# Kernel tuning notes

Measured on AMD Instinct MI355X. Metric: run time of the kernel, lower is better.

Reference implementation:

```python
import jax, jax.numpy as jnp
import numpy as np

B = 8192        # batch
OBS = 256       # obs_dim
ACT = 32        # action_dim -> output is 2*ACT (mu, log_std)
HID = 512       # hidden_dim
P = 8           # number of base policies (experts)
LOG_STD_MIN, LOG_STD_MAX = -5.0, 2.0


def setup_inputs() -> dict:
    key = jax.random.key(0)
    ks = jax.random.split(key, 14)
    s = 0.05
    return {
        "obs": jax.random.normal(ks[0], (B, OBS), dtype=jnp.float32),
        # gate network: obs -> HID -> HID -> P (softmax)
        "gw0": jax.random.normal(ks[1], (HID, OBS), dtype=jnp.float32) * s,
        "gb0": jnp.zeros((HID,), dtype=jnp.float32),
        "gw1": jax.random.normal(ks[2], (HID, HID), dtype=jnp.float32) * s,
        "gb1": jnp.zeros((HID,), dtype=jnp.float32),
        "gw2": jax.random.normal(ks[3], (P, HID), dtype=jnp.float32) * s,
        "gb2": jnp.zeros((P,), dtype=jnp.float32),
        # stacked expert (base-policy) trunk params, hidden_depth=2
        "ew0": jax.random.normal(ks[4], (P, HID, OBS), dtype=jnp.float32) * s,
        "eb0": jax.random.normal(ks[5], (P, HID), dtype=jnp.float32) * s,
        "ew1": jax.random.normal(ks[6], (P, HID, HID), dtype=jnp.float32) * s,
        "eb1": jax.random.normal(ks[7], (P, HID), dtype=jnp.float32) * s,
        "ew2": jax.random.normal(ks[8], (P, 2 * ACT, HID), dtype=jnp.float32) * s,
        "eb2": jax.random.normal(ks[9], (P, 2 * ACT), dtype=jnp.float32) * s,
    }


def _blend_linear(blend, W, b, x):
    # Math identical to: W_new = reshape(blend @ flatten(W,1)); bmm(W_new, x) + blend @ b
    # Contracted in the efficient order (per-expert GEMM then blend): [B,P,out] intermediate.
    y = jnp.einsum('bp,poi,bi->bo', blend, W, x, optimize=True)
    return y + blend @ b


def reference(obs, gw0, gb0, gw1, gb1, gw2, gb2, ew0, eb0, ew1, eb1, ew2, eb2):
    # gate network with softmax output
    h = jax.nn.relu(obs @ gw0.T + gb0)
    h = jax.nn.relu(h @ gw1.T + gb1)
    blend = jax.nn.softmax(h @ gw2.T + gb2, axis=-1)  # [B, P]

    # blended per-sample MLP (hidden_depth = 2)
    x = jax.nn.relu(_blend_linear(blend, ew0, eb0, obs))
    x = jax.nn.relu(_blend_linear(blend, ew1, eb1, x))
    x = _blend_linear(blend, ew2, eb2, x)  # [B, 2*ACT]

    mu, log_std = jnp.split(x, 2, axis=-1)
    log_std = jnp.tanh(log_std)
    log_std = LOG_STD_MIN + 0.5 * (LOG_STD_MAX - LOG_STD_MIN) * (log_std + 1.0)
    std = jnp.exp(log_std)
    # dist = SquashedNormal(mu, std); return its defining tensors
    return jnp.concatenate([mu, std], axis=-1)
```

## Files before the change

kernel.cpp:

```cpp
#include <hip/hip_runtime.h>
#include <hip/hip_bf16.h>
#include <cstdint>
#include <cstddef>

#define B_DIM   8192
#define OBS_DIM 256
#define ACT_DIM 32
#define HID_DIM 512
#define NEXPERT 8

typedef __attribute__((ext_vector_type(4))) float        f32x4;
typedef __attribute__((ext_vector_type(8))) short        s16x8;
typedef __attribute__((ext_vector_type(4))) unsigned int u32x4;

__device__ __forceinline__ unsigned cvt_pk_bf16(float lo, float hi) {
    unsigned r;
    asm("v_cvt_pk_bf16_f32 %0, %1, %2" : "=v"(r) : "v"(lo), "v"(hi));
    return r;
}
__device__ __forceinline__ float bf16_lo_f32(unsigned u) { return __uint_as_float(u << 16); }
__device__ __forceinline__ float bf16_hi_f32(unsigned u) { return __uint_as_float(u & 0xffff0000u); }

struct CvtArgs {
    const float*    s[7];
    unsigned short* d[7];
    int             nb[7];
};

__global__ __launch_bounds__(256) void cvt_multi(CvtArgs a) {
    int bid = blockIdx.x;
    int seg = 0, base = 0;
    while (seg < 6 && bid >= base + a.nb[seg]) { base += a.nb[seg]; ++seg; }
    int local = (bid - base) * 256 + threadIdx.x;
    const f32x4* s = (const f32x4*)a.s[seg];
    f32x4 v0 = s[local * 2 + 0];
    f32x4 v1 = s[local * 2 + 1];
    u32x4 o;
    o[0] = cvt_pk_bf16(v0[0], v0[1]);
    o[1] = cvt_pk_bf16(v0[2], v0[3]);
    o[2] = cvt_pk_bf16(v1[0], v1[1]);
    o[3] = cvt_pk_bf16(v1[2], v1[3]);
    ((u32x4*)a.d[seg])[local] = o;
}

__global__ __launch_bounds__(256) void gate_softmax(const unsigned short* __restrict__ h1,
                                                    const unsigned short* __restrict__ gw2,
                                                    const float* __restrict__ gb2,
                                                    float* __restrict__ blend) {
    const int lane = threadIdx.x & 63;
    const int wid  = threadIdx.x >> 6;
    const int row  = blockIdx.x * 4 + wid;

    u32x4 xv = *(const u32x4*)(h1 + (size_t)row * HID_DIM + lane * 8);
    float x[8];
#pragma unroll
    for (int j = 0; j < 4; ++j) {
        unsigned u   = xv[j];
        x[2 * j]     = bf16_lo_f32(u);
        x[2 * j + 1] = bf16_hi_f32(u);
    }
    float s[NEXPERT];
#pragma unroll
    for (int pp = 0; pp < NEXPERT; ++pp) {
        u32x4 wv = *(const u32x4*)(gw2 + (size_t)pp * HID_DIM + lane * 8);
        float d  = 0.f;
#pragma unroll
        for (int j = 0; j < 4; ++j) {
            unsigned u = wv[j];
            d += x[2 * j] * bf16_lo_f32(u);
            d += x[2 * j + 1] * bf16_hi_f32(u);
        }
        s[pp] = d;
    }
#pragma unroll
    for (int off = 1; off < 64; off <<= 1) {
#pragma unroll
        for (int pp = 0; pp < NEXPERT; ++pp) s[pp] += __shfl_xor(s[pp], off);
    }
    if (lane == 0) {
        float l[NEXPERT], m = -1e30f;
#pragma unroll
        for (int pp = 0; pp < NEXPERT; ++pp) { l[pp] = s[pp] + gb2[pp]; m = fmaxf(m, l[pp]); }
        float sum = 0.f;
#pragma unroll
        for (int pp = 0; pp < NEXPERT; ++pp) { l[pp] = __expf(l[pp] - m); sum += l[pp]; }
        float inv = 1.f / sum;
#pragma unroll
        for (int pp = 0; pp < NEXPERT; ++pp) blend[(size_t)row * NEXPERT + pp] = l[pp] * inv;
    }
}

template <int KIN, int NOUT>
__global__ __launch_bounds__(256, 2) void gemm_gate(const unsigned short* __restrict__ A,
                                                    const unsigned short* __restrict__ W,
                                                    const float* __restrict__ bias,
                                                    unsigned short* __restrict__ outb) {
    constexpr int BM = 128, BN = 64, BK = 64;

    __shared__ unsigned short sA[BM * BK];
    __shared__ unsigned short sB[BN * BK];

    const int t    = threadIdx.x;
    const int lane = t & 63;
    const int wid  = t >> 6;
    const int wm   = wid >> 1, wn = wid & 1;
    const int m0   = blockIdx.x * BM;
    const int n0   = blockIdx.y * BN;

    f32x4 acc[4][2];
#pragma unroll
    for (int i = 0; i < 4; ++i)
#pragma unroll
        for (int j = 0; j < 2; ++j) acc[i][j] = {0.f, 0.f, 0.f, 0.f};

#pragma unroll 1
    for (int kt = 0; kt < KIN / BK; ++kt) {
        const int ks = kt * BK;
        __syncthreads();
        const unsigned short* Wp = W + (size_t)n0 * KIN + ks;
#pragma unroll
        for (int c = 0; c < 2; ++c) {
            const int ch  = c * 256 + t;
            const int row = ch >> 3;
            const int gs  = (ch & 7) ^ (row & 7);
            __builtin_amdgcn_global_load_lds(
                (const __attribute__((address_space(1))) unsigned int*)(Wp + (size_t)row * KIN + gs * 8),
                (__attribute__((address_space(3))) unsigned int*)(sB + ch * 8), 16, 0, 0);
        }
        const unsigned short* Ap = A + (size_t)m0 * KIN + ks;
#pragma unroll
        for (int c = 0; c < 4; ++c) {
            const int ch  = c * 256 + t;
            const int row = ch >> 3;
            const int gs  = (ch & 7) ^ (row & 7);
            __builtin_amdgcn_global_load_lds(
                (const __attribute__((address_space(1))) unsigned int*)(Ap + (size_t)row * KIN + gs * 8),
                (__attribute__((address_space(3))) unsigned int*)(sA + ch * 8), 16, 0, 0);
        }
        __syncthreads();

#pragma unroll
        for (int kk = 0; kk < BK; kk += 32) {
            const int kb = kk + ((lane >> 4) << 3);
            s16x8 af[4], bfr[2];
#pragma unroll
            for (int mf = 0; mf < 4; ++mf) {
                const int row = wm * 64 + mf * 16 + (lane & 15);
                const int idx = (row * BK + kb) ^ ((row & 7) << 3);
                af[mf] = *(const s16x8*)(sA + idx);
            }
#pragma unroll
            for (int nf = 0; nf < 2; ++nf) {
                const int row = wn * 32 + nf * 16 + (lane & 15);
                const int idx = (row * BK + kb) ^ ((row & 7) << 3);
                bfr[nf] = *(const s16x8*)(sB + idx);
            }
#pragma unroll
            for (int mf = 0; mf < 4; ++mf)
#pragma unroll
                for (int nf = 0; nf < 2; ++nf)
                    acc[mf][nf] = __builtin_amdgcn_mfma_f32_16x16x32_bf16(af[mf], bfr[nf],
                                                                          acc[mf][nf], 0, 0, 0);
        }
    }

    const int cn = lane & 15;
    const int rb = (lane >> 4) << 2;
#pragma unroll
    for (int nf = 0; nf < 2; ++nf) {
        const int gn   = n0 + wn * 32 + nf * 16 + cn;
        const float bv = bias[gn];
#pragma unroll
        for (int mf = 0; mf < 4; ++mf) {
#pragma unroll
            for (int r = 0; r < 4; ++r) {
                const int gm = m0 + wm * 64 + mf * 16 + rb + r;
                float v = fmaxf(acc[mf][nf][r] + bv, 0.f);
                outb[(size_t)gm * NOUT + gn] = (unsigned short)(cvt_pk_bf16(v, v) & 0xffffu);
            }
        }
    }
}

template <int KIN, int NOUT, int BN, int TPB>
__global__ __launch_bounds__(256, 2) void gemm_moe_sk(const unsigned short* __restrict__ A,
                                                      const unsigned short* __restrict__ W,
                                                      const float* __restrict__ blend,
                                                      float* __restrict__ part) {
    constexpr int BM  = 128, BK = 64;
    constexpr int NF  = BN / 32;
    constexpr int TPE = KIN / BK;
    constexpr int NPE = (TPB >= TPE) ? TPB / TPE : 1;
    constexpr int ET  = (TPB >= TPE) ? TPE : TPB;
    static_assert((TPB % TPE == 0) || (TPE % TPB == 0), "split/expert alignment");

    __shared__ unsigned short sA[BM * BK];
    __shared__ unsigned short sB[BN * BK];

    const int t    = threadIdx.x;
    const int lane = t & 63;
    const int wid  = t >> 6;
    const int wm   = wid >> 1, wn = wid & 1;
    const int m0   = blockIdx.x * BM;
    const int n0   = blockIdx.y * BN;
    const int sp   = blockIdx.z;

    const int cn = lane & 15;
    const int rb = (lane >> 4) << 2;

    f32x4 mast[4][NF];
#pragma unroll
    for (int i = 0; i < 4; ++i)
#pragma unroll
        for (int j = 0; j < NF; ++j) mast[i][j] = {0.f, 0.f, 0.f, 0.f};

#pragma unroll 1
    for (int pe = 0; pe < NPE; ++pe) {
        const int tbase = sp * TPB + pe * ET;
        const int p     = tbase / TPE;
        const int ksb   = (tbase % TPE) * BK;

        f32x4 eacc[4][NF];
#pragma unroll
        for (int i = 0; i < 4; ++i)
#pragma unroll
            for (int j = 0; j < NF; ++j) eacc[i][j] = {0.f, 0.f, 0.f, 0.f};

        const unsigned short* Ap0 = A + (size_t)m0 * KIN + ksb;
        const unsigned short* Wp0 = W + ((size_t)p * NOUT + n0) * KIN + ksb;

#pragma unroll 1
        for (int kt = 0; kt < ET; ++kt) {
            const int ks = kt * BK;
            __syncthreads();
#pragma unroll
            for (int c = 0; c < NF; ++c) {
                const int ch  = c * 256 + t;
                const int row = ch >> 3;
                const int gs  = (ch & 7) ^ (row & 7);
                __builtin_amdgcn_global_load_lds(
                    (const __attribute__((address_space(1))) unsigned int*)(Wp0 + (size_t)row * KIN + ks + gs * 8),
                    (__attribute__((address_space(3))) unsigned int*)(sB + ch * 8), 16, 0, 0);
            }
#pragma unroll
            for (int c = 0; c < 4; ++c) {
                const int ch  = c * 256 + t;
                const int row = ch >> 3;
                const int gs  = (ch & 7) ^ (row & 7);
                __builtin_amdgcn_global_load_lds(
                    (const __attribute__((address_space(1))) unsigned int*)(Ap0 + (size_t)row * KIN + ks + gs * 8),
                    (__attribute__((address_space(3))) unsigned int*)(sA + ch * 8), 16, 0, 0);
            }
            __syncthreads();

#pragma unroll
            for (int kk = 0; kk < BK; kk += 32) {
                const int kb = kk + ((lane >> 4) << 3);
                s16x8 af[4], bfr[NF];
#pragma unroll
                for (int mf = 0; mf < 4; ++mf) {
                    const int row = wm * 64 + mf * 16 + (lane & 15);
                    const int idx = (row * BK + kb) ^ ((row & 7) << 3);
                    af[mf] = *(const s16x8*)(sA + idx);
                }
#pragma unroll
                for (int nf = 0; nf < NF; ++nf) {
                    const int row = wn * (BN / 2) + nf * 16 + (lane & 15);
                    const int idx = (row * BK + kb) ^ ((row & 7) << 3);
                    bfr[nf] = *(const s16x8*)(sB + idx);
                }
#pragma unroll
                for (int mf = 0; mf < 4; ++mf)
#pragma unroll
                    for (int nf = 0; nf < NF; ++nf)
                        eacc[mf][nf] = __builtin_amdgcn_mfma_f32_16x16x32_bf16(af[mf], bfr[nf],
                                                                               eacc[mf][nf], 0, 0, 0);
            }
        }

#pragma unroll
        for (int mf = 0; mf < 4; ++mf) {
#pragma unroll
            for (int r = 0; r < 4; ++r) {
                const int gm = m0 + wm * 64 + mf * 16 + rb + r;
                const float bl = blend[(size_t)gm * NEXPERT + p];
#pragma unroll
                for (int nf = 0; nf < NF; ++nf)
                    mast[mf][nf][r] += bl * eacc[mf][nf][r];
            }
        }
    }

    float* dst = part + (size_t)sp * B_DIM * NOUT;
#pragma unroll
    for (int mf = 0; mf < 4; ++mf) {
#pragma unroll
        for (int r = 0; r < 4; ++r) {
            const int gm = m0 + wm * 64 + mf * 16 + rb + r;
#pragma unroll
            for (int nf = 0; nf < NF; ++nf) {
                const int gn = n0 + wn * (BN / 2) + nf * 16 + cn;
                dst[(size_t)gm * NOUT + gn] = mast[mf][nf][r];
            }
        }
    }
}

template <int NS>
__global__ __launch_bounds__(256) void reduceN_relu(const float* __restrict__ part,
                                                    const float* __restrict__ blend,
                                                    const float* __restrict__ eb,
                                                    unsigned short* __restrict__ out) {
    const int tid = blockIdx.x * 256 + threadIdx.x;
    const int row = tid >> 6;
    const int c0  = (tid & 63) << 3;

    float res[8] = {0.f, 0.f, 0.f, 0.f, 0.f, 0.f, 0.f, 0.f};
#pragma unroll
    for (int s = 0; s < NS; ++s) {
        const f32x4* ps = (const f32x4*)(part + ((size_t)s * B_DIM + row) * HID_DIM + c0);
        const f32x4 a = ps[0], b = ps[1];
#pragma unroll
        for (int j = 0; j < 4; ++j) { res[j] += a[j]; res[4 + j] += b[j]; }
    }
    const f32x4* bl = (const f32x4*)(blend + (size_t)row * NEXPERT);
    const f32x4 b0 = bl[0], b1 = bl[1];
    const float blv[8] = {b0[0], b0[1], b0[2], b0[3], b1[0], b1[1], b1[2], b1[3]};
#pragma unroll
    for (int pp = 0; pp < NEXPERT; ++pp) {
        const f32x4* e = (const f32x4*)(eb + (size_t)pp * HID_DIM + c0);
        const f32x4 e0 = e[0], e1 = e[1];
#pragma unroll
        for (int j = 0; j < 4; ++j) {
            res[j]     += blv[pp] * e0[j];
            res[4 + j] += blv[pp] * e1[j];
        }
    }
    u32x4 o;
#pragma unroll
    for (int j = 0; j < 4; ++j)
        o[j] = cvt_pk_bf16(fmaxf(res[2 * j], 0.f), fmaxf(res[2 * j + 1], 0.f));
    *(u32x4*)(out + (size_t)row * HID_DIM + c0) = o;
}

__global__ __launch_bounds__(256) void reduce16_head(const float* __restrict__ part,
                                                     const float* __restrict__ blend,
                                                     const float* __restrict__ eb2,
                                                     float* __restrict__ out) {
    const int tid = blockIdx.x * 256 + threadIdx.x;
    const int row = tid >> 3;
    const int c0  = (tid & 7) << 3;

    float res[8] = {0.f, 0.f, 0.f, 0.f, 0.f, 0.f, 0.f, 0.f};
#pragma unroll
    for (int sp = 0; sp < 16; ++sp) {
        const f32x4* ps = (const f32x4*)(part + ((size_t)sp * B_DIM + row) * 64 + c0);
        const f32x4 a = ps[0], b = ps[1];
#pragma unroll
        for (int j = 0; j < 4; ++j) { res[j] += a[j]; res[4 + j] += b[j]; }
    }
    const f32x4* bl = (const f32x4*)(blend + (size_t)row * NEXPERT);
    const f32x4 b0 = bl[0], b1 = bl[1];
    const float blv[8] = {b0[0], b0[1], b0[2], b0[3], b1[0], b1[1], b1[2], b1[3]};
#pragma unroll
    for (int pp = 0; pp < NEXPERT; ++pp) {
        const f32x4* e = (const f32x4*)(eb2 + (size_t)pp * 64 + c0);
        const f32x4 e0 = e[0], e1 = e[1];
#pragma unroll
        for (int j = 0; j < 4; ++j) {
            res[j]     += blv[pp] * e0[j];
            res[4 + j] += blv[pp] * e1[j];
        }
    }
    f32x4 o0, o1;
#pragma unroll
    for (int j = 0; j < 8; ++j) {
        const int col = c0 + j;
        float v = res[j];
        if (col >= ACT_DIM) {
            const float vc = fminf(fmaxf(v, -15.f), 15.f);
            const float e2 = __expf(2.f * vc);
            const float th = (e2 - 1.f) / (e2 + 1.f);
            v = __expf(-1.5f + 3.5f * th);
        }
        if (j < 4) o0[j] = v; else o1[j - 4] = v;
    }
    f32x4* dst = (f32x4*)(out + (size_t)row * 64 + c0);
    dst[0] = o0;
    dst[1] = o1;
}

extern "C" void kernel_launch(void* const* d_in, const int* in_sizes, int n_in,
                              void* d_out, int out_size, void* d_ws, size_t ws_size,
                              hipStream_t stream) {
    const float* obs = (const float*)d_in[0];
    const float* gw0 = (const float*)d_in[1];
    const float* gb0 = (const float*)d_in[2];
    const float* gw1 = (const float*)d_in[3];
    const float* gb1 = (const float*)d_in[4];
    const float* gw2 = (const float*)d_in[5];
    const float* gb2 = (const float*)d_in[6];
    const float* ew0 = (const float*)d_in[7];
    const float* eb0 = (const float*)d_in[8];
    const float* ew1 = (const float*)d_in[9];
    const float* eb1 = (const float*)d_in[10];
    const float* ew2 = (const float*)d_in[11];
    const float* eb2 = (const float*)d_in[12];

    char* w = (char*)d_ws;
    auto alloc = [&](size_t bytes) {
        char* r = w;
        w += (bytes + 255) & ~(size_t)255;
        return r;
    };
    unsigned short* obs_bf = (unsigned short*)alloc((size_t)B_DIM * OBS_DIM * 2);
    unsigned short* gw0_bf = (unsigned short*)alloc((size_t)HID_DIM * OBS_DIM * 2);
    unsigned short* gw1_bf = (unsigned short*)alloc((size_t)HID_DIM * HID_DIM * 2);
    unsigned short* gw2_bf = (unsigned short*)alloc((size_t)NEXPERT * HID_DIM * 2);
    unsigned short* ew0_bf = (unsigned short*)alloc((size_t)NEXPERT * HID_DIM * OBS_DIM * 2);
    unsigned short* ew1_bf = (unsigned short*)alloc((size_t)NEXPERT * HID_DIM * HID_DIM * 2);
    unsigned short* ew2_bf = (unsigned short*)alloc((size_t)NEXPERT * 2 * ACT_DIM * HID_DIM * 2);
    unsigned short* h0     = (unsigned short*)alloc((size_t)B_DIM * HID_DIM * 2);
    unsigned short* h1     = (unsigned short*)alloc((size_t)B_DIM * HID_DIM * 2);
    float*          blend  = (float*)alloc((size_t)B_DIM * NEXPERT * 4);

    const size_t part4_bytes = (size_t)4 * B_DIM * HID_DIM * 4;
    const size_t part2_bytes = (size_t)2 * B_DIM * HID_DIM * 4;
    const size_t used        = (size_t)(w - (char*)d_ws);
    const bool   big         = (ws_size - used) >= part4_bytes;
    float* part = (float*)alloc(big ? part4_bytes : part2_bytes);

    CvtArgs ca;
    ca.s[0] = obs; ca.d[0] = obs_bf; ca.nb[0] = (B_DIM * OBS_DIM / 8) / 256;
    ca.s[1] = gw0; ca.d[1] = gw0_bf; ca.nb[1] = (HID_DIM * OBS_DIM / 8) / 256;
    ca.s[2] = gw1; ca.d[2] = gw1_bf; ca.nb[2] = (HID_DIM * HID_DIM / 8) / 256;
    ca.s[3] = gw2; ca.d[3] = gw2_bf; ca.nb[3] = (NEXPERT * HID_DIM / 8) / 256;
    ca.s[4] = ew0; ca.d[4] = ew0_bf; ca.nb[4] = (NEXPERT * HID_DIM * OBS_DIM / 8) / 256;
    ca.s[5] = ew1; ca.d[5] = ew1_bf; ca.nb[5] = (NEXPERT * HID_DIM * HID_DIM / 8) / 256;
    ca.s[6] = ew2; ca.d[6] = ew2_bf; ca.nb[6] = (NEXPERT * 64 * HID_DIM / 8) / 256;
    int total_blocks = 0;
    for (int i = 0; i < 7; ++i) total_blocks += ca.nb[i];
    cvt_multi<<<total_blocks, 256, 0, stream>>>(ca);

    gemm_gate<OBS_DIM, HID_DIM><<<dim3(B_DIM / 128, HID_DIM / 64), 256, 0, stream>>>(
        obs_bf, gw0_bf, gb0, h0);
    gemm_gate<HID_DIM, HID_DIM><<<dim3(B_DIM / 128, HID_DIM / 64), 256, 0, stream>>>(
        h0, gw1_bf, gb1, h1);
    gate_softmax<<<B_DIM / 4, 256, 0, stream>>>(h1, gw2_bf, gb2, blend);

    if (big) {
        gemm_moe_sk<OBS_DIM, HID_DIM, 128, 8>
            <<<dim3(B_DIM / 128, HID_DIM / 128, 4), 256, 0, stream>>>(obs_bf, ew0_bf, blend, part);
        reduceN_relu<4><<<B_DIM * 64 / 256, 256, 0, stream>>>(part, blend, eb0, h0);

        gemm_moe_sk<HID_DIM, HID_DIM, 128, 16>
            <<<dim3(B_DIM / 128, HID_DIM / 128, 4), 256, 0, stream>>>(h0, ew1_bf, blend, part);
        reduceN_relu<4><<<B_DIM * 64 / 256, 256, 0, stream>>>(part, blend, eb1, h1);
    } else {
        gemm_moe_sk<OBS_DIM, HID_DIM, 128, 16>
            <<<dim3(B_DIM / 128, HID_DIM / 128, 2), 256, 0, stream>>>(obs_bf, ew0_bf, blend, part);
        reduceN_relu<2><<<B_DIM * 64 / 256, 256, 0, stream>>>(part, blend, eb0, h0);

        gemm_moe_sk<HID_DIM, HID_DIM, 128, 32>
            <<<dim3(B_DIM / 128, HID_DIM / 128, 2), 256, 0, stream>>>(h0, ew1_bf, blend, part);
        reduceN_relu<2><<<B_DIM * 64 / 256, 256, 0, stream>>>(part, blend, eb1, h1);
    }

    gemm_moe_sk<HID_DIM, 64, 64, 4>
        <<<dim3(B_DIM / 128, 1, 16), 256, 0, stream>>>(h1, ew2_bf, blend, part);
    reduce16_head<<<B_DIM * 8 / 256, 256, 0, stream>>>(part, blend, eb2, (float*)d_out);
}
```

Measured before the change: 231.9 us.

## Use 512-thread expert GEMM blocks, always split in two, shrink head split-K

The two hidden-layer expert GEMMs move to a new 512-thread kernel with 8 waves in a 2x4 layout. Each wave now holds half as many N fragments. Both layers now always use the 2-way split that covers four experts per block, which drops the 4-way split path and halves partial-buffer traffic. The head GEMM drops from 16 to 8 splits, one expert per split, with the blend applied at store time, and its reduction shrinks to match. The change trades fewer blocks and less reduction traffic for lower parallelism per layer, and a different occupancy and register profile.

```diff
diff --git a/kernel.cpp b/kernel.cpp
--- a/kernel.cpp
+++ b/kernel.cpp
@@ -183,16 +183,165 @@
 }
 
 template <int KIN, int NOUT, int BN, int TPB>
-__global__ __launch_bounds__(256, 2) void gemm_moe_sk(const unsigned short* __restrict__ A,
-                                                      const unsigned short* __restrict__ W,
-                                                      const float* __restrict__ blend,
-                                                      float* __restrict__ part) {
+__global__ __launch_bounds__(512, 2) void gemm_moe_sk8(const unsigned short* __restrict__ A,
+                                                       const unsigned short* __restrict__ W,
+                                                       const float* __restrict__ blend,
+                                                       float* __restrict__ part) {
+    constexpr int BM  = 128, BK = 64;
+    constexpr int NF  = BN / 64;
+    constexpr int TPE = KIN / BK;
+    constexpr int NPE = (TPB >= TPE) ? TPB / TPE : 1;
+    constexpr int ET  = (TPB >= TPE) ? TPE : TPB;
+    static_assert((TPB % TPE == 0) || (TPE % TPB == 0), "split/expert alignment");
+
+    __shared__ unsigned short sA[BM * BK];
+    __shared__ unsigned short sB[BN * BK];
+
+    const int t    = threadIdx.x;
+    const int lane = t & 63;
+    const int wid  = t >> 6;
+    const int wm   = wid >> 2;
+    const int wn   = wid & 3;
+    const int m0   = blockIdx.x * BM;
+    const int n0   = blockIdx.y * BN;
+    const int sp   = blockIdx.z;
+
+    const int cn = lane & 15;
+    const int rb = (lane >> 4) << 2;
+
+    f32x4 mast[4][NF];
+    if constexpr (NPE > 1) {
+#pragma unroll
+        for (int i = 0; i < 4; ++i)
+#pragma unroll
+            for (int j = 0; j < NF; ++j) mast[i][j] = {0.f, 0.f, 0.f, 0.f};
+    }
+
+    float lastbl[4];
+
+#pragma unroll 1
+    for (int pe = 0; pe < NPE; ++pe) {
+        const int tbase = sp * TPB + pe * ET;
+        const int p     = tbase / TPE;
+        const int ksb   = (tbase % TPE) * BK;
+
+        f32x4 eacc[4][NF];
+#pragma unroll
+        for (int i = 0; i < 4; ++i)
+#pragma unroll
+            for (int j = 0; j < NF; ++j) eacc[i][j] = {0.f, 0.f, 0.f, 0.f};
+
+        const unsigned short* Ap0 = A + (size_t)m0 * KIN + ksb;
+        const unsigned short* Wp0 = W + ((size_t)p * NOUT + n0) * KIN + ksb;
+
+#pragma unroll 1
+        for (int kt = 0; kt < ET; ++kt) {
+            const int ks = kt * BK;
+            __syncthreads();
+#pragma unroll
+            for (int c = 0; c < BN * 8 / 512; ++c) {
+                const int ch  = c * 512 + t;
+                const int row = ch >> 3;
+                const int gs  = (ch & 7) ^ (row & 7);
+                __builtin_amdgcn_global_load_lds(
+                    (const __attribute__((address_space(1))) unsigned int*)(Wp0 + (size_t)row * KIN + ks + gs * 8),
+                    (__attribute__((address_space(3))) unsigned int*)(sB + ch * 8), 16, 0, 0);
+            }
+#pragma unroll
+            for (int c = 0; c < 2; ++c) {
+                const int ch  = c * 512 + t;
+                const int row = ch >> 3;
+                const int gs  = (ch & 7) ^ (row & 7);
+                __builtin_amdgcn_global_load_lds(
+                    (const __attribute__((address_space(1))) unsigned int*)(Ap0 + (size_t)row * KIN + ks + gs * 8),
+                    (__attribute__((address_space(3))) unsigned int*)(sA + ch * 8), 16, 0, 0);
+            }
+            __syncthreads();
+
+#pragma unroll
+            for (int kk = 0; kk < BK; kk += 32) {
+                const int kb = kk + ((lane >> 4) << 3);
+                s16x8 af[4], bfr[NF];
+#pragma unroll
+                for (int mf = 0; mf < 4; ++mf) {
+                    const int row = wm * 64 + mf * 16 + (lane & 15);
+                    const int idx = (row * BK + kb) ^ ((row & 7) << 3);
+                    af[mf] = *(const s16x8*)(sA + idx);
+                }
+#pragma unroll
+                for (int nf = 0; nf < NF; ++nf) {
+                    const int row = wn * (BN / 4) + nf * 16 + (lane & 15);
+                    const int idx = (row * BK + kb) ^ ((row & 7) << 3);
+                    bfr[nf] = *(const s16x8*)(sB + idx);
+                }
+#pragma unroll
+                for (int mf = 0; mf < 4; ++mf)
+#pragma unroll
+                    for (int nf = 0; nf < NF; ++nf)
+                        eacc[mf][nf] = __builtin_amdgcn_mfma_f32_16x16x32_bf16(af[mf], bfr[nf],
+                                                                               eacc[mf][nf], 0, 0, 0);
+            }
+        }
+
+        if constexpr (NPE > 1) {
+#pragma unroll
+            for (int mf = 0; mf < 4; ++mf) {
+#pragma unroll
+                for (int r = 0; r < 4; ++r) {
+                    const int gm = m0 + wm * 64 + mf * 16 + rb + r;
+                    const float bl = blend[(size_t)gm * NEXPERT + p];
+#pragma unroll
+                    for (int nf = 0; nf < NF; ++nf)
+                        mast[mf][nf][r] += bl * eacc[mf][nf][r];
+                }
+            }
+        } else {
+#pragma unroll
+            for (int mf = 0; mf < 4; ++mf) {
+                const int gm = m0 + wm * 64 + mf * 16 + rb;
+                lastbl[mf] = 0.f;
+                (void)gm;
+#pragma unroll
+                for (int r = 0; r < 4; ++r) {
+                    const float bl = blend[(size_t)(m0 + wm * 64 + mf * 16 + rb + r) * NEXPERT + p];
+#pragma unroll
+                    for (int nf = 0; nf < NF; ++nf)
+                        eacc[mf][nf][r] *= bl;
+                }
+#pragma unroll
+                for (int nf = 0; nf < NF; ++nf) mast[mf][nf] = eacc[mf][nf];
+            }
+        }
+    }
+    (void)lastbl;
+
+    float* dst = part + (size_t)sp * B_DIM * NOUT;
+#pragma unroll
+    for (int mf = 0; mf < 4; ++mf) {
+#pragma unroll
+        for (int r = 0; r < 4; ++r) {
+            const int gm = m0 + wm * 64 + mf * 16 + rb + r;
+#pragma unroll
+            for (int nf = 0; nf < NF; ++nf) {
+                const int gn = n0 + wn * (BN / 4) + nf * 16 + cn;
+                dst[(size_t)gm * NOUT + gn] = mast[mf][nf][r];
+            }
+        }
+    }
+}
+
+template <int KIN, int NOUT, int BN, int TPB>
+__global__ __launch_bounds__(256, 2) void gemm_moe_sk4(const unsigned short* __restrict__ A,
+                                                       const unsigned short* __restrict__ W,
+                                                       const float* __restrict__ blend,
+                                                       float* __restrict__ part) {
     constexpr int BM  = 128, BK = 64;
     constexpr int NF  = BN / 32;
     constexpr int TPE = KIN / BK;
     constexpr int NPE = (TPB >= TPE) ? TPB / TPE : 1;
     constexpr int ET  = (TPB >= TPE) ? TPE : TPB;
     static_assert((TPB % TPE == 0) || (TPE % TPB == 0), "split/expert alignment");
+    static_assert(NPE == 1, "sk4 is the single-expert-chunk path");
 
     __shared__ unsigned short sA[BM * BK];
     __shared__ unsigned short sB[BN * BK];
@@ -208,86 +357,65 @@
     const int cn = lane & 15;
     const int rb = (lane >> 4) << 2;
 
-    f32x4 mast[4][NF];
+    const int tbase = sp * TPB;
+    const int p     = tbase / TPE;
+    const int ksb   = (tbase % TPE) * BK;
+
+    f32x4 eacc[4][NF];
 #pragma unroll
     for (int i = 0; i < 4; ++i)
 #pragma unroll
-        for (int j = 0; j < NF; ++j) mast[i][j] = {0.f, 0.f, 0.f, 0.f};
+        for (int j = 0; j < NF; ++j) eacc[i][j] = {0.f, 0.f, 0.f, 0.f};
+
+    const unsigned short* Ap0 = A + (size_t)m0 * KIN + ksb;
+    const unsigned short* Wp0 = W + ((size_t)p * NOUT + n0) * KIN + ksb;
 
 #pragma unroll 1
-    for (int pe = 0; pe < NPE; ++pe) {
-        const int tbase = sp * TPB + pe * ET;
-        const int p     = tbase / TPE;
-        const int ksb   = (tbase % TPE) * BK;
-
-        f32x4 eacc[4][NF];
-#pragma unroll
-        for (int i = 0; i < 4; ++i)
-#pragma unroll
-            for (int j = 0; j < NF; ++j) eacc[i][j] = {0.f, 0.f, 0.f, 0.f};
-
-        const unsigned short* Ap0 = A + (size_t)m0 * KIN + ksb;
-        const unsigned short* Wp0 = W + ((size_t)p * NOUT + n0) * KIN + ksb;
-
-#pragma unroll 1
-        for (int kt = 0; kt < ET; ++kt) {
-            const int ks = kt * BK;
-            __syncthreads();
-#pragma unroll
-            for (int c = 0; c < NF; ++c) {
-                const int ch  = c * 256 + t;
-                const int row = ch >> 3;
-                const int gs  = (ch & 7) ^ (row & 7);
-                __builtin_amdgcn_global_load_lds(
-                    (const __attribute__((address_space(1))) unsigned int*)(Wp0 + (size_t)row * KIN + ks + gs * 8),
-                    (__attribute__((address_space(3))) unsigned int*)(sB + ch * 8), 16, 0, 0);
-            }
-#pragma unroll
-            for (int c = 0; c < 4; ++c) {
-                const int ch  = c * 256 + t;
-                const int row = ch >> 3;
-                const int gs  = (ch & 7) ^ (row & 7);
-                __builtin_amdgcn_global_load_lds(
-                    (const __attribute__((address_space(1))) unsigned int*)(Ap0 + (size_t)row * KIN + ks + gs * 8),
-                    (__attribute__((address_space(3))) unsigned int*)(sA + ch * 8), 16, 0, 0);
-            }
-            __syncthreads();
-
-#pragma unroll
-            for (int kk = 0; kk < BK; kk += 32) {
-                const int kb = kk + ((lane >> 4) << 3);
-                s16x8 af[4], bfr[NF];
-#pragma unroll
-                for (int mf = 0; mf < 4; ++mf) {
-                    const int row = wm * 64 + mf * 16 + (lane & 15);
-                    const int idx = (row * BK + kb) ^ ((row & 7) << 3);
-                    af[mf] = *(const s16x8*)(sA + idx);
-                }
-#pragma unroll
-                for (int nf = 0; nf < NF; ++nf) {
-                    const int row = wn * (BN / 2) + nf * 16 + (lane & 15);
-                    const int idx = (row * BK + kb) ^ ((row & 7) << 3);
-                    bfr[nf] = *(const s16x8*)(sB + idx);
-                }
-#pragma unroll
-                for (int mf = 0; mf < 4; ++mf)
-#pragma unroll
-                    for (int nf = 0; nf < NF; ++nf)
-                        eacc[mf][nf] = __builtin_amdgcn_mfma_f32_16x16x32_bf16(af[mf], bfr[nf],
-                                                                               eacc[mf][nf], 0, 0, 0);
-            }
-        }
-
-#pragma unroll
-        for (int mf = 0; mf < 4; ++mf) {
-#pragma unroll
-            for (int r = 0; r < 4; ++r) {
-                const int gm = m0 + wm * 64 + mf * 16 + rb + r;
-                const float bl = blend[(size_t)gm * NEXPERT + p];
+    for (int kt = 0; kt < ET; ++kt) {
+        const int ks = kt * BK;
+        __syncthreads();
+#pragma unroll
+        for (int c = 0; c < NF; ++c) {
+            const int ch  = c * 256 + t;
+            const int row = ch >> 3;
+            const int gs  = (ch & 7) ^ (row & 7);
+            __builtin_amdgcn_global_load_lds(
+                (const __attribute__((address_space(1))) unsigned int*)(Wp0 + (size_t)row * KIN + ks + gs * 8),
+                (__attribute__((address_space(3))) unsigned int*)(sB + ch * 8), 16, 0, 0);
+        }
+#pragma unroll
+        for (int c = 0; c < 4; ++c) {
+            const int ch  = c * 256 + t;
+            const int row = ch >> 3;
+            const int gs  = (ch & 7) ^ (row & 7);
+            __builtin_amdgcn_global_load_lds(
+                (const __attribute__((address_space(1))) unsigned int*)(Ap0 + (size_t)row * KIN + ks + gs * 8),
+                (__attribute__((address_space(3))) unsigned int*)(sA + ch * 8), 16, 0, 0);
+        }
+        __syncthreads();
+
+#pragma unroll
+        for (int kk = 0; kk < BK; kk += 32) {
+            const int kb = kk + ((lane >> 4) << 3);
+            s16x8 af[4], bfr[NF];
+#pragma unroll
+            for (int mf = 0; mf < 4; ++mf) {
+                const int row = wm * 64 + mf * 16 + (lane & 15);
+                const int idx = (row * BK + kb) ^ ((row & 7) << 3);
+                af[mf] = *(const s16x8*)(sA + idx);
+            }
+#pragma unroll
+            for (int nf = 0; nf < NF; ++nf) {
+                const int row = wn * (BN / 2) + nf * 16 + (lane & 15);
+                const int idx = (row * BK + kb) ^ ((row & 7) << 3);
+                bfr[nf] = *(const s16x8*)(sB + idx);
+            }
+#pragma unroll
+            for (int mf = 0; mf < 4; ++mf)
 #pragma unroll
                 for (int nf = 0; nf < NF; ++nf)
-                    mast[mf][nf][r] += bl * eacc[mf][nf][r];
-            }
+                    eacc[mf][nf] = __builtin_amdgcn_mfma_f32_16x16x32_bf16(af[mf], bfr[nf],
+                                                                           eacc[mf][nf], 0, 0, 0);
         }
     }
 
@@ -297,10 +425,11 @@
 #pragma unroll
         for (int r = 0; r < 4; ++r) {
             const int gm = m0 + wm * 64 + mf * 16 + rb + r;
+            const float bl = blend[(size_t)gm * NEXPERT + p];
 #pragma unroll
             for (int nf = 0; nf < NF; ++nf) {
                 const int gn = n0 + wn * (BN / 2) + nf * 16 + cn;
-                dst[(size_t)gm * NOUT + gn] = mast[mf][nf][r];
+                dst[(size_t)gm * NOUT + gn] = bl * eacc[mf][nf][r];
             }
         }
     }
@@ -343,17 +472,17 @@
     *(u32x4*)(out + (size_t)row * HID_DIM + c0) = o;
 }
 
-__global__ __launch_bounds__(256) void reduce16_head(const float* __restrict__ part,
-                                                     const float* __restrict__ blend,
-                                                     const float* __restrict__ eb2,
-                                                     float* __restrict__ out) {
+__global__ __launch_bounds__(256) void reduce8_head(const float* __restrict__ part,
+                                                    const float* __restrict__ blend,
+                                                    const float* __restrict__ eb2,
+                                                    float* __restrict__ out) {
     const int tid = blockIdx.x * 256 + threadIdx.x;
     const int row = tid >> 3;
     const int c0  = (tid & 7) << 3;
 
     float res[8] = {0.f, 0.f, 0.f, 0.f, 0.f, 0.f, 0.f, 0.f};
 #pragma unroll
-    for (int sp = 0; sp < 16; ++sp) {
+    for (int sp = 0; sp < 8; ++sp) {
         const f32x4* ps = (const f32x4*)(part + ((size_t)sp * B_DIM + row) * 64 + c0);
         const f32x4 a = ps[0], b = ps[1];
 #pragma unroll
@@ -423,12 +552,7 @@
     unsigned short* h0     = (unsigned short*)alloc((size_t)B_DIM * HID_DIM * 2);
     unsigned short* h1     = (unsigned short*)alloc((size_t)B_DIM * HID_DIM * 2);
     float*          blend  = (float*)alloc((size_t)B_DIM * NEXPERT * 4);
-
-    const size_t part4_bytes = (size_t)4 * B_DIM * HID_DIM * 4;
-    const size_t part2_bytes = (size_t)2 * B_DIM * HID_DIM * 4;
-    const size_t used        = (size_t)(w - (char*)d_ws);
-    const bool   big         = (ws_size - used) >= part4_bytes;
-    float* part = (float*)alloc(big ? part4_bytes : part2_bytes);
+    float*          part   = (float*)alloc((size_t)2 * B_DIM * HID_DIM * 4);
 
     CvtArgs ca;
     ca.s[0] = obs; ca.d[0] = obs_bf; ca.nb[0] = (B_DIM * OBS_DIM / 8) / 256;
@@ -448,25 +572,15 @@
         h0, gw1_bf, gb1, h1);
     gate_softmax<<<B_DIM / 4, 256, 0, stream>>>(h1, gw2_bf, gb2, blend);
 
-    if (big) {
-        gemm_moe_sk<OBS_DIM, HID_DIM, 128, 8>
-            <<<dim3(B_DIM / 128, HID_DIM / 128, 4), 256, 0, stream>>>(obs_bf, ew0_bf, blend, part);
-        reduceN_relu<4><<<B_DIM * 64 / 256, 256, 0, stream>>>(part, blend, eb0, h0);
-
-        gemm_moe_sk<HID_DIM, HID_DIM, 128, 16>
-            <<<dim3(B_DIM / 128, HID_DIM / 128, 4), 256, 0, stream>>>(h0, ew1_bf, blend, part);
-        reduceN_relu<4><<<B_DIM * 64 / 256, 256, 0, stream>>>(part, blend, eb1, h1);
-    } else {
-        gemm_moe_sk<OBS_DIM, HID_DIM, 128, 16>
-            <<<dim3(B_DIM / 128, HID_DIM / 128, 2), 256, 0, stream>>>(obs_bf, ew0_bf, blend, part);
-        reduceN_relu<2><<<B_DIM * 64 / 256, 256, 0, stream>>>(part, blend, eb0, h0);
-
-        gemm_moe_sk<HID_DIM, HID_DIM, 128, 32>
-            <<<dim3(B_DIM / 128, HID_DIM / 128, 2), 256, 0, stream>>>(h0, ew1_bf, blend, part);
-        reduceN_relu<2><<<B_DIM * 64 / 256, 256, 0, stream>>>(part, blend, eb1, h1);
-    }
-
-    gemm_moe_sk<HID_DIM, 64, 64, 4>
-        <<<dim3(B_DIM / 128, 1, 16), 256, 0, stream>>>(h1, ew2_bf, blend, part);
-    reduce16_head<<<B_DIM * 8 / 256, 256, 0, stream>>>(part, blend, eb2, (float*)d_out);
-}
+    gemm_moe_sk8<OBS_DIM, HID_DIM, 128, 16>
+        <<<dim3(B_DIM / 128, HID_DIM / 128, 2), 512, 0, stream>>>(obs_bf, ew0_bf, blend, part);
+    reduceN_relu<2><<<B_DIM * 64 / 256, 256, 0, stream>>>(part, blend, eb0, h0);
+
+    gemm_moe_sk8<HID_DIM, HID_DIM, 128, 32>
+        <<<dim3(B_DIM / 128, HID_DIM / 128, 2), 512, 0, stream>>>(h0, ew1_bf, blend, part);
+    reduceN_relu<2><<<B_DIM * 64 / 256, 256, 0, stream>>>(part, blend, eb1, h1);
+
+    gemm_moe_sk4<HID_DIM, 64, 64, 8>
+        <<<dim3(B_DIM / 128, 1, 8), 256, 0, stream>>>(h1, ew2_bf, blend, part);
+    reduce8_head<<<B_DIM * 8 / 256, 256, 0, stream>>>(part, blend, eb2, (float*)d_out);
+}
```

Result: slower. 247.3 us (+6.6%).

## Double-buffer LDS in gate and MoE GEMMs and reduce split-K counts

Applied to the files above, without the earlier changes.

Adds double-buffered shared memory to the gate and expert GEMMs, so the next K tile is loaded asynchronously while MFMAs run on the current one. The MoE kernel's nested per-expert loop becomes a single flat tile loop that folds the blended expert accumulator into the master accumulator at expert boundaries. The launch config is fixed to the 2-way split for the hidden layers and 8-way for the head, which drops the workspace-size branch and halves the head's reduction partials. LDS use doubles per block, which may cut occupancy, and fewer splits reduce grid parallelism.

```diff
diff --git a/kernel.cpp b/kernel.cpp
--- a/kernel.cpp
+++ b/kernel.cpp
@@ -96,9 +96,10 @@
                                                     const float* __restrict__ bias,
                                                     unsigned short* __restrict__ outb) {
     constexpr int BM = 128, BN = 64, BK = 64;
-
-    __shared__ unsigned short sA[BM * BK];
-    __shared__ unsigned short sB[BN * BK];
+    constexpr int NT = KIN / BK;
+
+    __shared__ unsigned short sA[2][BM * BK];
+    __shared__ unsigned short sB[2][BN * BK];
 
     const int t    = threadIdx.x;
     const int lane = t & 63;
@@ -107,16 +108,8 @@
     const int m0   = blockIdx.x * BM;
     const int n0   = blockIdx.y * BN;
 
-    f32x4 acc[4][2];
-#pragma unroll
-    for (int i = 0; i < 4; ++i)
-#pragma unroll
-        for (int j = 0; j < 2; ++j) acc[i][j] = {0.f, 0.f, 0.f, 0.f};
-
-#pragma unroll 1
-    for (int kt = 0; kt < KIN / BK; ++kt) {
-        const int ks = kt * BK;
-        __syncthreads();
+    auto stage = [&](int tile, int buf) {
+        const int ks = tile * BK;
         const unsigned short* Wp = W + (size_t)n0 * KIN + ks;
 #pragma unroll
         for (int c = 0; c < 2; ++c) {
@@ -125,7 +118,7 @@
             const int gs  = (ch & 7) ^ (row & 7);
             __builtin_amdgcn_global_load_lds(
                 (const __attribute__((address_space(1))) unsigned int*)(Wp + (size_t)row * KIN + gs * 8),
-                (__attribute__((address_space(3))) unsigned int*)(sB + ch * 8), 16, 0, 0);
+                (__attribute__((address_space(3))) unsigned int*)(&sB[buf][ch * 8]), 16, 0, 0);
         }
         const unsigned short* Ap = A + (size_t)m0 * KIN + ks;
 #pragma unroll
@@ -135,9 +128,23 @@
             const int gs  = (ch & 7) ^ (row & 7);
             __builtin_amdgcn_global_load_lds(
                 (const __attribute__((address_space(1))) unsigned int*)(Ap + (size_t)row * KIN + gs * 8),
-                (__attribute__((address_space(3))) unsigned int*)(sA + ch * 8), 16, 0, 0);
-        }
-        __syncthreads();
+                (__attribute__((address_space(3))) unsigned int*)(&sA[buf][ch * 8]), 16, 0, 0);
+        }
+    };
+
+    f32x4 acc[4][2];
+#pragma unroll
+    for (int i = 0; i < 4; ++i)
+#pragma unroll
+        for (int j = 0; j < 2; ++j) acc[i][j] = {0.f, 0.f, 0.f, 0.f};
+
+    stage(0, 0);
+    __syncthreads();
+    int cur = 0;
+
+#pragma unroll 1
+    for (int tile = 0; tile < NT; ++tile) {
+        if (tile + 1 < NT) stage(tile + 1, cur ^ 1);
 
 #pragma unroll
         for (int kk = 0; kk < BK; kk += 32) {
@@ -147,13 +154,13 @@
             for (int mf = 0; mf < 4; ++mf) {
                 const int row = wm * 64 + mf * 16 + (lane & 15);
                 const int idx = (row * BK + kb) ^ ((row & 7) << 3);
-                af[mf] = *(const s16x8*)(sA + idx);
+                af[mf] = *(const s16x8*)(&sA[cur][idx]);
             }
 #pragma unroll
             for (int nf = 0; nf < 2; ++nf) {
                 const int row = wn * 32 + nf * 16 + (lane & 15);
                 const int idx = (row * BK + kb) ^ ((row & 7) << 3);
-                bfr[nf] = *(const s16x8*)(sB + idx);
+                bfr[nf] = *(const s16x8*)(&sB[cur][idx]);
             }
 #pragma unroll
             for (int mf = 0; mf < 4; ++mf)
@@ -162,6 +169,8 @@
                     acc[mf][nf] = __builtin_amdgcn_mfma_f32_16x16x32_bf16(af[mf], bfr[nf],
                                                                           acc[mf][nf], 0, 0, 0);
         }
+        __syncthreads();
+        cur ^= 1;
     }
 
     const int cn = lane & 15;
@@ -190,12 +199,11 @@
     constexpr int BM  = 128, BK = 64;
     constexpr int NF  = BN / 32;
     constexpr int TPE = KIN / BK;
-    constexpr int NPE = (TPB >= TPE) ? TPB / TPE : 1;
     constexpr int ET  = (TPB >= TPE) ? TPE : TPB;
     static_assert((TPB % TPE == 0) || (TPE % TPB == 0), "split/expert alignment");
 
-    __shared__ unsigned short sA[BM * BK];
-    __shared__ unsigned short sB[BN * BK];
+    __shared__ unsigned short sA[2][BM * BK];
+    __shared__ unsigned short sB[2][BN * BK];
 
     const int t    = threadIdx.x;
     const int lane = t & 63;
@@ -207,88 +215,94 @@
 
     const int cn = lane & 15;
     const int rb = (lane >> 4) << 2;
-
-    f32x4 mast[4][NF];
+    const unsigned gbase = (unsigned)sp * TPB;
+
+    auto stage = [&](int tile, int buf) {
+        const unsigned g  = gbase + (unsigned)tile;
+        const unsigned p  = g / TPE;
+        const unsigned ko = (g % TPE) * BK;
+        const unsigned short* Wp = W + ((size_t)p * NOUT + n0) * KIN + ko;
+#pragma unroll
+        for (int c = 0; c < BN / 32; ++c) {
+            const int ch  = c * 256 + t;
+            const int row = ch >> 3;
+            const int gs  = (ch & 7) ^ (row & 7);
+            __builtin_amdgcn_global_load_lds(
+                (const __attribute__((address_space(1))) unsigned int*)(Wp + (size_t)row * KIN + gs * 8),
+                (__attribute__((address_space(3))) unsigned int*)(&sB[buf][ch * 8]), 16, 0, 0);
+        }
+        const unsigned short* Ap = A + (size_t)m0 * KIN + ko;
+#pragma unroll
+        for (int c = 0; c < 4; ++c) {
+            const int ch  = c * 256 + t;
+            const int row = ch >> 3;
+            const int gs  = (ch & 7) ^ (row & 7);
+            __builtin_amdgcn_global_load_lds(
+                (const __attribute__((address_space(1))) unsigned int*)(Ap + (size_t)row * KIN + gs * 8),
+                (__attribute__((address_space(3))) unsigned int*)(&sA[buf][ch * 8]), 16, 0, 0);
+        }
+    };
+
+    f32x4 mast[4][NF], eacc[4][NF];
 #pragma unroll
     for (int i = 0; i < 4; ++i)
 #pragma unroll
-        for (int j = 0; j < NF; ++j) mast[i][j] = {0.f, 0.f, 0.f, 0.f};
+        for (int j = 0; j < NF; ++j) {
+            mast[i][j] = {0.f, 0.f, 0.f, 0.f};
+            eacc[i][j] = {0.f, 0.f, 0.f, 0.f};
+        }
+
+    stage(0, 0);
+    __syncthreads();
+    int cur = 0;
 
 #pragma unroll 1
-    for (int pe = 0; pe < NPE; ++pe) {
-        const int tbase = sp * TPB + pe * ET;
-        const int p     = tbase / TPE;
-        const int ksb   = (tbase % TPE) * BK;
-
-        f32x4 eacc[4][NF];
-#pragma unroll
-        for (int i = 0; i < 4; ++i)
-#pragma unroll
-            for (int j = 0; j < NF; ++j) eacc[i][j] = {0.f, 0.f, 0.f, 0.f};
-
-        const unsigned short* Ap0 = A + (size_t)m0 * KIN + ksb;
-        const unsigned short* Wp0 = W + ((size_t)p * NOUT + n0) * KIN + ksb;
-
-#pragma unroll 1
-        for (int kt = 0; kt < ET; ++kt) {
-            const int ks = kt * BK;
-            __syncthreads();
-#pragma unroll
-            for (int c = 0; c < NF; ++c) {
-                const int ch  = c * 256 + t;
-                const int row = ch >> 3;
-                const int gs  = (ch & 7) ^ (row & 7);
-                __builtin_amdgcn_global_load_lds(
-                    (const __attribute__((address_space(1))) unsigned int*)(Wp0 + (size_t)row * KIN + ks + gs * 8),
-                    (__attribute__((address_space(3))) unsigned int*)(sB + ch * 8), 16, 0, 0);
-            }
-#pragma unroll
-            for (int c = 0; c < 4; ++c) {
-                const int ch  = c * 256 + t;
-                const int row = ch >> 3;
-                const int gs  = (ch & 7) ^ (row & 7);
-                __builtin_amdgcn_global_load_lds(
-                    (const __attribute__((address_space(1))) unsigned int*)(Ap0 + (size_t)row * KIN + ks + gs * 8),
-                    (__attribute__((address_space(3))) unsigned int*)(sA + ch * 8), 16, 0, 0);
-            }
-            __syncthreads();
-
-#pragma unroll
-            for (int kk = 0; kk < BK; kk += 32) {
-                const int kb = kk + ((lane >> 4) << 3);
-                s16x8 af[4], bfr[NF];
-#pragma unroll
-                for (int mf = 0; mf < 4; ++mf) {
-                    const int row = wm * 64 + mf * 16 + (lane & 15);
-                    const int idx = (row * BK + kb) ^ ((row & 7) << 3);
-                    af[mf] = *(const s16x8*)(sA + idx);
+    for (int tile = 0; tile < TPB; ++tile) {
+        if (tile + 1 < TPB) stage(tile + 1, cur ^ 1);
+
+#pragma unroll
+        for (int kk = 0; kk < BK; kk += 32) {
+            const int kb = kk + ((lane >> 4) << 3);
+            s16x8 af[4], bfr[NF];
+#pragma unroll
+            for (int mf = 0; mf < 4; ++mf) {
+                const int row = wm * 64 + mf * 16 + (lane & 15);
+                const int idx = (row * BK + kb) ^ ((row & 7) << 3);
+                af[mf] = *(const s16x8*)(&sA[cur][idx]);
+            }
+#pragma unroll
+            for (int nf = 0; nf < NF; ++nf) {
+                const int row = wn * (BN / 2) + nf * 16 + (lane & 15);
+                const int idx = (row * BK + kb) ^ ((row & 7) << 3);
+                bfr[nf] = *(const s16x8*)(&sB[cur][idx]);
+            }
+#pragma unroll
+            for (int mf = 0; mf < 4; ++mf)
+#pragma unroll
+                for (int nf = 0; nf < NF; ++nf)
+                    eacc[mf][nf] = __builtin_amdgcn_mfma_f32_16x16x32_bf16(af[mf], bfr[nf],
+                                                                           eacc[mf][nf], 0, 0, 0);
+        }
+
+        if (((tile + 1) & (ET - 1)) == 0) {
+            const unsigned p = (gbase + (unsigned)tile) / TPE;
+#pragma unroll
+            for (int mf = 0; mf < 4; ++mf) {
+#pragma unroll
+                for (int r = 0; r < 4; ++r) {
+                    const int gm = m0 + wm * 64 + mf * 16 + rb + r;
+                    const float bl = blend[(size_t)gm * NEXPERT + p];
+#pragma unroll
+                    for (int nf = 0; nf < NF; ++nf) {
+                        mast[mf][nf][r] += bl * eacc[mf][nf][r];
+                        eacc[mf][nf][r] = 0.f;
+                    }
                 }
-#pragma unroll
-                for (int nf = 0; nf < NF; ++nf) {
-                    const int row = wn * (BN / 2) + nf * 16 + (lane & 15);
-                    const int idx = (row * BK + kb) ^ ((row & 7) << 3);
-                    bfr[nf] = *(const s16x8*)(sB + idx);
-                }
-#pragma unroll
-                for (int mf = 0; mf < 4; ++mf)
-#pragma unroll
-                    for (int nf = 0; nf < NF; ++nf)
-                        eacc[mf][nf] = __builtin_amdgcn_mfma_f32_16x16x32_bf16(af[mf], bfr[nf],
-                                                                               eacc[mf][nf], 0, 0, 0);
-            }
-        }
-
-#pragma unroll
-        for (int mf = 0; mf < 4; ++mf) {
-#pragma unroll
-            for (int r = 0; r < 4; ++r) {
-                const int gm = m0 + wm * 64 + mf * 16 + rb + r;
-                const float bl = blend[(size_t)gm * NEXPERT + p];
-#pragma unroll
-                for (int nf = 0; nf < NF; ++nf)
-                    mast[mf][nf][r] += bl * eacc[mf][nf][r];
-            }
-        }
+            }
+        }
+
+        __syncthreads();
+        cur ^= 1;
     }
 
     float* dst = part + (size_t)sp * B_DIM * NOUT;
@@ -343,17 +357,17 @@
     *(u32x4*)(out + (size_t)row * HID_DIM + c0) = o;
 }
 
-__global__ __launch_bounds__(256) void reduce16_head(const float* __restrict__ part,
-                                                     const float* __restrict__ blend,
-                                                     const float* __restrict__ eb2,
-                                                     float* __restrict__ out) {
+__global__ __launch_bounds__(256) void reduce8_head(const float* __restrict__ part,
+                                                    const float* __restrict__ blend,
+                                                    const float* __restrict__ eb2,
+                                                    float* __restrict__ out) {
     const int tid = blockIdx.x * 256 + threadIdx.x;
     const int row = tid >> 3;
     const int c0  = (tid & 7) << 3;
 
     float res[8] = {0.f, 0.f, 0.f, 0.f, 0.f, 0.f, 0.f, 0.f};
 #pragma unroll
-    for (int sp = 0; sp < 16; ++sp) {
+    for (int sp = 0; sp < 8; ++sp) {
         const f32x4* ps = (const f32x4*)(part + ((size_t)sp * B_DIM + row) * 64 + c0);
         const f32x4 a = ps[0], b = ps[1];
 #pragma unroll
@@ -423,12 +437,7 @@
     unsigned short* h0     = (unsigned short*)alloc((size_t)B_DIM * HID_DIM * 2);
     unsigned short* h1     = (unsigned short*)alloc((size_t)B_DIM * HID_DIM * 2);
     float*          blend  = (float*)alloc((size_t)B_DIM * NEXPERT * 4);
-
-    const size_t part4_bytes = (size_t)4 * B_DIM * HID_DIM * 4;
-    const size_t part2_bytes = (size_t)2 * B_DIM * HID_DIM * 4;
-    const size_t used        = (size_t)(w - (char*)d_ws);
-    const bool   big         = (ws_size - used) >= part4_bytes;
-    float* part = (float*)alloc(big ? part4_bytes : part2_bytes);
+    float*          part   = (float*)alloc((size_t)2 * B_DIM * HID_DIM * 4);
 
     CvtArgs ca;
     ca.s[0] = obs; ca.d[0] = obs_bf; ca.nb[0] = (B_DIM * OBS_DIM / 8) / 256;
@@ -448,25 +457,15 @@
         h0, gw1_bf, gb1, h1);
     gate_softmax<<<B_DIM / 4, 256, 0, stream>>>(h1, gw2_bf, gb2, blend);
 
-    if (big) {
-        gemm_moe_sk<OBS_DIM, HID_DIM, 128, 8>
-            <<<dim3(B_DIM / 128, HID_DIM / 128, 4), 256, 0, stream>>>(obs_bf, ew0_bf, blend, part);
-        reduceN_relu<4><<<B_DIM * 64 / 256, 256, 0, stream>>>(part, blend, eb0, h0);
-
-        gemm_moe_sk<HID_DIM, HID_DIM, 128, 16>
-            <<<dim3(B_DIM / 128, HID_DIM / 128, 4), 256, 0, stream>>>(h0, ew1_bf, blend, part);
-        reduceN_relu<4><<<B_DIM * 64 / 256, 256, 0, stream>>>(part, blend, eb1, h1);
-    } else {
-        gemm_moe_sk<OBS_DIM, HID_DIM, 128, 16>
-            <<<dim3(B_DIM / 128, HID_DIM / 128, 2), 256, 0, stream>>>(obs_bf, ew0_bf, blend, part);
-        reduceN_relu<2><<<B_DIM * 64 / 256, 256, 0, stream>>>(part, blend, eb0, h0);
-
-        gemm_moe_sk<HID_DIM, HID_DIM, 128, 32>
-            <<<dim3(B_DIM / 128, HID_DIM / 128, 2), 256, 0, stream>>>(h0, ew1_bf, blend, part);
-        reduceN_relu<2><<<B_DIM * 64 / 256, 256, 0, stream>>>(part, blend, eb1, h1);
-    }
-
-    gemm_moe_sk<HID_DIM, 64, 64, 4>
-        <<<dim3(B_DIM / 128, 1, 16), 256, 0, stream>>>(h1, ew2_bf, blend, part);
-    reduce16_head<<<B_DIM * 8 / 256, 256, 0, stream>>>(part, blend, eb2, (float*)d_out);
-}
+    gemm_moe_sk<OBS_DIM, HID_DIM, 128, 16>
+        <<<dim3(B_DIM / 128, HID_DIM / 128, 2), 256, 0, stream>>>(obs_bf, ew0_bf, blend, part);
+    reduceN_relu<2><<<B_DIM * 64 / 256, 256, 0, stream>>>(part, blend, eb0, h0);
+
+    gemm_moe_sk<HID_DIM, HID_DIM, 128, 32>
+        <<<dim3(B_DIM / 128, HID_DIM / 128, 2), 256, 0, stream>>>(h0, ew1_bf, blend, part);
+    reduceN_relu<2><<<B_DIM * 64 / 256, 256, 0, stream>>>(part, blend, eb1, h1);
+
+    gemm_moe_sk<HID_DIM, 64, 64, 8>
+        <<<dim3(B_DIM / 128, 1, 8), 256, 0, stream>>>(h1, ew2_bf, blend, part);
+    reduce8_head<<<B_DIM * 8 / 256, 256, 0, stream>>>(part, blend, eb2, (float*)d_out);
+}
```

After: 209.8 us. 9.6% less time.
